# Performance work log

Measured on AMD Instinct MI355X. Metric: run time of the kernel, lower is better.

The kernel has to match this reference:

```python
import jax, jax.numpy as jnp
import numpy as np

N = 50000      # nodes
E = 800000     # edges (before self loops)
IN = 128       # input_dim
H1, C1 = 4, 64   # conv1 heads, per-head channels (concat -> 256)
H2, C2 = 1, 64   # conv2 heads, per-head channels (concat=False -> 64)
EPS_BN = 1e-5
NEG_SLOPE = 0.2


def setup_inputs() -> dict:
    key = jax.random.key(0)
    ks = jax.random.split(key, 20)
    s = 0.05
    d = {}
    d["x"] = jax.random.normal(ks[0], (N, IN), dtype=jnp.float32)
    d["edge_index"] = jax.random.randint(ks[1], (2, E), 0, N, dtype=jnp.int32)
    # GATConv 1: lin weight [IN, H1*C1], att vectors [H1, C1], bias [H1*C1]
    d["W1"] = jax.random.normal(ks[2], (IN, H1 * C1), dtype=jnp.float32) * s
    d["a1_src"] = jax.random.normal(ks[3], (H1, C1), dtype=jnp.float32) * s
    d["a1_dst"] = jax.random.normal(ks[4], (H1, C1), dtype=jnp.float32) * s
    d["b1"] = jnp.zeros((H1 * C1,), jnp.float32)
    # GATConv 2 (concat=False): lin weight [H1*C1, H2*C2]
    d["W2"] = jax.random.normal(ks[5], (H1 * C1, H2 * C2), dtype=jnp.float32) * s
    d["a2_src"] = jax.random.normal(ks[6], (H2, C2), dtype=jnp.float32) * s
    d["a2_dst"] = jax.random.normal(ks[7], (H2, C2), dtype=jnp.float32) * s
    d["b2"] = jnp.zeros((C2,), jnp.float32)
    # projection Linear(output_dim -> input_dim)
    d["Wp"] = jax.random.normal(ks[8], (C2, IN), dtype=jnp.float32) * s
    d["bp"] = jnp.zeros((IN,), jnp.float32)
    # BatchNorm affine params
    d["g1"] = jnp.ones((H1 * C1,), jnp.float32); d["be1"] = jnp.zeros((H1 * C1,), jnp.float32)
    d["g2"] = jnp.ones((C2,), jnp.float32);      d["be2"] = jnp.zeros((C2,), jnp.float32)
    d["g3"] = jnp.ones((IN,), jnp.float32);      d["be3"] = jnp.zeros((IN,), jnp.float32)
    return d


def batch_norm(x, gamma, beta):
    mu = jnp.mean(x, axis=0, keepdims=True)
    var = jnp.var(x, axis=0, keepdims=True)
    return (x - mu) * jax.lax.rsqrt(var + EPS_BN) * gamma + beta


def gat_conv(x, src, dst, W, a_src, a_dst, bias, heads, out_ch, concat):
    n = x.shape[0]
    h = (x @ W).reshape(n, heads, out_ch)            # [N,H,C]
    alpha_s = jnp.einsum('nhc,hc->nh', h, a_src)     # [N,H]
    alpha_d = jnp.einsum('nhc,hc->nh', h, a_dst)
    e = jax.nn.leaky_relu(alpha_s[src] + alpha_d[dst], NEG_SLOPE)  # [E',H]
    # segment softmax over edges sharing the same destination node
    m = jax.ops.segment_max(e, dst, num_segments=n)
    m = jnp.where(jnp.isfinite(m), m, 0.0)
    ex = jnp.exp(e - m[dst])
    den = jax.ops.segment_sum(ex, dst, num_segments=n)
    alpha = ex / (den[dst] + 1e-16)                  # [E',H]
    msg = alpha[:, :, None] * h[src]                 # [E',H,C]
    out = jax.ops.segment_sum(msg, dst, num_segments=n)  # [N,H,C]
    if concat:
        out = out.reshape(n, heads * out_ch)
    else:
        out = out.mean(axis=1)
    return out + bias


def reference(x, edge_index, W1, a1_src, a1_dst, b1, W2, a2_src, a2_dst, b2,
              Wp, bp, g1, be1, g2, be2, g3, be3):
    n = x.shape[0]
    # PyG GATConv default add_self_loops=True
    loops = jnp.arange(n, dtype=edge_index.dtype)
    src = jnp.concatenate([edge_index[0], loops])
    dst = jnp.concatenate([edge_index[1], loops])
    h = gat_conv(x, src, dst, W1, a1_src, a1_dst, b1, H1, C1, True)
    h = jax.nn.elu(batch_norm(h, g1, be1))
    # dropout is a no-op in eval mode
    h = gat_conv(h, src, dst, W2, a2_src, a2_dst, b2, H2, C2, False)
    h = jax.nn.elu(batch_norm(h, g2, be2))
    h = h @ Wp + bp
    return batch_norm(h, g3, be3)
```

## Files before the change

kernel.cpp:

```cpp
#include <hip/hip_runtime.h>
#include <cstdint>
#include <cstddef>

#define NEG_SLOPE 0.2f
#define EPS_BN 1e-5f

typedef __bf16 bf16x8 __attribute__((ext_vector_type(8)));
typedef float  f32x4  __attribute__((ext_vector_type(4)));
typedef float  f32x2  __attribute__((ext_vector_type(2)));
typedef unsigned short ushort_t;

static __device__ __forceinline__ float lrelu(float x){ return x > 0.f ? x : NEG_SLOPE * x; }
static __device__ __forceinline__ float elu(float x){ return x > 0.f ? x : __expf(x) - 1.f; }

static __device__ __forceinline__ ushort_t f2bf(float f){
  unsigned u = __float_as_uint(f);
  u += 0x7fffu + ((u >> 16) & 1u);
  return (ushort_t)(u >> 16);
}
static __device__ __forceinline__ void unpk(unsigned u, float& lo, float& hi){
  lo = __uint_as_float(u << 16);
  hi = __uint_as_float(u & 0xffff0000u);
}
static __device__ __forceinline__ f32x2 unpk2(unsigned u){
  f32x2 r;
  r.x = __uint_as_float(u << 16);
  r.y = __uint_as_float(u & 0xffff0000u);
  return r;
}

union BF8 { bf16x8 v; ushort_t u[8]; };

static inline int ceil_div(int a, int b){ return (a + b - 1) / b; }


static __device__ void packW_body(const float* W, ushort_t* Wp, int K, int Nn, int idx){
  int lane = idx & 63;
  int rest = idx >> 6;
  int KS = K >> 5;
  int s = rest % KS, t = rest / KS;
  int n  = t * 16 + (lane & 15);
  int k0 = s * 32 + (lane >> 4) * 8;
  ushort_t tmp[8];
  #pragma unroll
  for(int j = 0; j < 8; j++) tmp[j] = f2bf(W[(size_t)(k0 + j) * Nn + n]);
  uint4 pk;
  pk.x = tmp[0] | ((unsigned)tmp[1] << 16);
  pk.y = tmp[2] | ((unsigned)tmp[3] << 16);
  pk.z = tmp[4] | ((unsigned)tmp[5] << 16);
  pk.w = tmp[6] | ((unsigned)tmp[7] << 16);
  *reinterpret_cast<uint4*>(Wp + (size_t)idx * 8) = pk;
}

__global__ void init_kernel(unsigned* __restrict__ zbase, int ztotal,
                            const float* __restrict__ W1, const float* __restrict__ W2,
                            const float* __restrict__ W3, ushort_t* __restrict__ W1p,
                            ushort_t* __restrict__ W2p, ushort_t* __restrict__ W3p){
  int b = blockIdx.x;
  if(b < 28){
    int idx = b * 256 + threadIdx.x;
    if(idx < 4096)       packW_body(W1, W1p, 128, 256, idx);
    else if(idx < 6144)  packW_body(W2, W2p, 256, 64,  idx - 4096);
    else if(idx < 7168)  packW_body(W3, W3p, 64,  128, idx - 6144);
  } else {
    int i = (b - 28) * 256 + threadIdx.x;
    if(i < ztotal) zbase[i] = 0u;
  }
}


template<int K, int NT, int AMODE, int H>
static __device__ __forceinline__ void gemm_body(int bx, const void* __restrict__ Asrc,
                                                 const ushort_t* __restrict__ Bp,
                                                 ushort_t* __restrict__ C, int M,
                                                 const float* __restrict__ scale,
                                                 const float* __restrict__ shift,
                                                 const float* __restrict__ a_src,
                                                 const float* __restrict__ a_dst,
                                                 float* __restrict__ as_,
                                                 float* __restrict__ ad_){
  constexpr int KS = K >> 5;
  int lane = threadIdx.x & 63, wv = threadIdx.x >> 6;
  int row0 = bx * 64 + wv * 16;
  int mi = lane & 15, q = lane >> 4;
  int arow = row0 + mi; if(arow > M - 1) arow = M - 1;
  const bf16x8* bbase = reinterpret_cast<const bf16x8*>(Bp) + lane;
  f32x4 acc[NT] = {};
  #pragma unroll
  for(int s = 0; s < KS; s++){
    BF8 cv;
    if(AMODE == 0){
      const float* ap = (const float*)Asrc + (size_t)arow * K + s * 32 + q * 8;
      float4 u0 = *reinterpret_cast<const float4*>(ap);
      float4 u1 = *reinterpret_cast<const float4*>(ap + 4);
      cv.u[0] = f2bf(u0.x); cv.u[1] = f2bf(u0.y); cv.u[2] = f2bf(u0.z); cv.u[3] = f2bf(u0.w);
      cv.u[4] = f2bf(u1.x); cv.u[5] = f2bf(u1.y); cv.u[6] = f2bf(u1.z); cv.u[7] = f2bf(u1.w);
    } else {
      const ushort_t* ap = (const ushort_t*)Asrc + (size_t)arow * K + s * 32 + q * 8;
      uint4 u = *reinterpret_cast<const uint4*>(ap);
      int c0 = s * 32 + q * 8;
      float4 sc0 = *reinterpret_cast<const float4*>(scale + c0);
      float4 sc1 = *reinterpret_cast<const float4*>(scale + c0 + 4);
      float4 sh0 = *reinterpret_cast<const float4*>(shift + c0);
      float4 sh1 = *reinterpret_cast<const float4*>(shift + c0 + 4);
      float a, b;
      unpk(u.x, a, b); cv.u[0] = f2bf(elu(a * sc0.x + sh0.x)); cv.u[1] = f2bf(elu(b * sc0.y + sh0.y));
      unpk(u.y, a, b); cv.u[2] = f2bf(elu(a * sc0.z + sh0.z)); cv.u[3] = f2bf(elu(b * sc0.w + sh0.w));
      unpk(u.z, a, b); cv.u[4] = f2bf(elu(a * sc1.x + sh1.x)); cv.u[5] = f2bf(elu(b * sc1.y + sh1.y));
      unpk(u.w, a, b); cv.u[6] = f2bf(elu(a * sc1.z + sh1.z)); cv.u[7] = f2bf(elu(b * sc1.w + sh1.w));
    }
    bf16x8 af = cv.v;
    #pragma unroll
    for(int t = 0; t < NT; t++){
      bf16x8 bfr = bbase[((size_t)t * KS + s) * 64];
      acc[t] = __builtin_amdgcn_mfma_f32_16x16x32_bf16(af, bfr, acc[t], 0, 0, 0);
    }
  }
  #pragma unroll
  for(int t = 0; t < NT; t++){
    #pragma unroll
    for(int r = 0; r < 4; r++){
      int gr = row0 + q * 4 + r;
      if(gr < M) C[(size_t)gr * (NT * 16) + t * 16 + mi] = f2bf(acc[t][r]);
    }
  }
  if(H > 0){
    #pragma unroll
    for(int hh = 0; hh < H; hh++){
      #pragma unroll
      for(int r = 0; r < 4; r++){
        float ps = 0.f, pd = 0.f;
        #pragma unroll
        for(int tt = 0; tt < 4; tt++){
          int t = hh * 4 + tt;
          float av = acc[t][r];
          int c = t * 16 + mi;
          ps += av * a_src[c];
          pd += av * a_dst[c];
        }
        #pragma unroll
        for(int off = 1; off < 16; off <<= 1){
          ps += __shfl_xor(ps, off);
          pd += __shfl_xor(pd, off);
        }
        int gr = row0 + q * 4 + r;
        if(mi == 0 && gr < M){
          as_[(size_t)gr * H + hh] = ps;
          ad_[(size_t)gr * H + hh] = pd;
        }
      }
    }
  }
}

template<int K, int NT, int AMODE, int H>
__global__ __launch_bounds__(256) void gemm_kernel(const void* __restrict__ Asrc,
                                                   const ushort_t* __restrict__ Bp,
                                                   ushort_t* __restrict__ C, int M,
                                                   const float* __restrict__ scale,
                                                   const float* __restrict__ shift,
                                                   const float* __restrict__ a_src,
                                                   const float* __restrict__ a_dst,
                                                   float* __restrict__ as_,
                                                   float* __restrict__ ad_){
  gemm_body<K, NT, AMODE, H>(blockIdx.x, Asrc, Bp, C, M, scale, shift, a_src, a_dst, as_, ad_);
}

__global__ __launch_bounds__(256) void hist_gemm1_kernel(int GB, const int* __restrict__ ei,
                                                         int* __restrict__ deg, int E, int N,
                                                         const float* __restrict__ x,
                                                         const ushort_t* __restrict__ W1p,
                                                         ushort_t* __restrict__ h1b,
                                                         const float* __restrict__ a1s,
                                                         const float* __restrict__ a1d,
                                                         float* __restrict__ as_,
                                                         float* __restrict__ ad_){
  int b = blockIdx.x;
  if(b < GB){
    gemm_body<128, 16, 0, 4>(b, x, W1p, h1b, N, nullptr, nullptr, a1s, a1d, as_, ad_);
  } else {
    int e = (b - GB) * 256 + threadIdx.x;
    if(e < E + N){
      int d = (e < E) ? ei[E + e] : (e - E);
      atomicAdd(&deg[d], 1);
    }
  }
}


__global__ __launch_bounds__(256) void scan1_kernel(const int* __restrict__ deg, int* __restrict__ rowptr,
                                                    int* __restrict__ partials,
                                                    unsigned* __restrict__ tick, int n){
  int t = threadIdx.x, lane = t & 63, wv = t >> 6;
  int base = blockIdx.x * 2048 + t * 8;
  int v[8]; int run = 0;
  #pragma unroll
  for(int k = 0; k < 8; k++){ int i = base + k; v[k] = (i < n) ? deg[i] : 0; run += v[k]; }
  int sc = run;
  #pragma unroll
  for(int off = 1; off < 64; off <<= 1){
    int u = __shfl_up(sc, off);
    if(lane >= off) sc += u;
  }
  __shared__ int wtot[4], woff[4];
  __shared__ bool slast;
  if(lane == 63) wtot[wv] = sc;
  __syncthreads();
  if(t == 0){
    int a = 0;
    #pragma unroll
    for(int i = 0; i < 4; i++){ woff[i] = a; a += wtot[i]; }
    partials[blockIdx.x] = a;
  }
  __syncthreads();
  int excl = (sc - run) + woff[wv];
  #pragma unroll
  for(int k = 0; k < 8; k++){
    int i = base + k;
    if(i < n){ rowptr[i] = excl; excl += v[k]; }
  }
  if(t == 0){
    __threadfence();
    slast = (atomicAdd(tick, 1u) == (unsigned)(gridDim.x - 1));
  }
  __syncthreads();
  if(slast && t < 64){
    int nb = gridDim.x;
    int pv = (t < nb) ? atomicAdd(&partials[t], 0) : 0;
    int psc = pv;
    #pragma unroll
    for(int off = 1; off < 64; off <<= 1){
      int u = __shfl_up(psc, off);
      if(t >= off) psc += u;
    }
    if(t < nb) partials[t] = psc - pv;
  }
}

__global__ void scatter_kernel(const int* __restrict__ ei, int* __restrict__ rowptr,
                               const int* __restrict__ part, int* __restrict__ col, int E, int N){
  int e = blockIdx.x * 256 + threadIdx.x;
  if(e >= E + N) return;
  int s, d;
  if(e < E){ s = ei[e]; d = ei[E + e]; } else { s = e - E; d = e - E; }
  int pos = atomicAdd(&rowptr[d], 1) + part[d >> 11];
  col[pos] = s;
}


__global__ __launch_bounds__(256) void gat_agg4_kernel(const ushort_t* __restrict__ hfeat,
                                                       const float* __restrict__ as_,
                                                       const float* __restrict__ ad_,
                                                       const int* __restrict__ rowptr,
                                                       const int* __restrict__ part,
                                                       const int* __restrict__ col,
                                                       const float* __restrict__ bias,
                                                       ushort_t* __restrict__ out, int N){
  int wid = threadIdx.x >> 6, lane = threadIdx.x & 63;
  int n = blockIdx.x * 4 + wid;
  if(n > N - 1) n = N - 1;
  int start = n ? rowptr[n - 1] + part[(n - 1) >> 11] : 0;
  int end   = rowptr[n] + part[n >> 11];
  int g = lane >> 5, l = lane & 31, hidx = l >> 3;
  float adh = ad_[(size_t)n * 4 + hidx];
  float den = 0.f;
  f32x2 acc2[4] = {};
  auto body = [&](int j){
    int s = col[j];
    float w = __expf(lrelu(as_[(size_t)s * 4 + hidx] + adh));
    uint4 u = *reinterpret_cast<const uint4*>(hfeat + (size_t)s * 256 + 8 * l);
    den += w;
    acc2[0] += unpk2(u.x) * w;
    acc2[1] += unpk2(u.y) * w;
    acc2[2] += unpk2(u.z) * w;
    acc2[3] += unpk2(u.w) * w;
  };
  int j = start + g;
  for(; j + 6 < end; j += 8){ body(j); body(j + 2); body(j + 4); body(j + 6); }
  for(; j < end; j += 2) body(j);
  den += __shfl_xor(den, 32);
  #pragma unroll
  for(int k = 0; k < 4; k++){
    acc2[k].x += __shfl_xor(acc2[k].x, 32);
    acc2[k].y += __shfl_xor(acc2[k].y, 32);
  }
  float dinv = 1.f / (den + 1e-16f);
  int cbase = 8 * l + g * 4;
  f32x2 p0 = g ? acc2[2] : acc2[0];
  f32x2 p1 = g ? acc2[3] : acc2[1];
  ushort_t o0 = f2bf(p0.x * dinv + bias[cbase + 0]);
  ushort_t o1 = f2bf(p0.y * dinv + bias[cbase + 1]);
  ushort_t o2 = f2bf(p1.x * dinv + bias[cbase + 2]);
  ushort_t o3 = f2bf(p1.y * dinv + bias[cbase + 3]);
  uint2 pk; pk.x = o0 | ((unsigned)o1 << 16); pk.y = o2 | ((unsigned)o3 << 16);
  *reinterpret_cast<uint2*>(out + (size_t)n * 256 + cbase) = pk;
}


__global__ __launch_bounds__(256) void gat_agg1_kernel(const ushort_t* __restrict__ hfeat,
                                                       const float* __restrict__ as_,
                                                       const float* __restrict__ ad_,
                                                       const int* __restrict__ rowptr,
                                                       const int* __restrict__ part,
                                                       const int* __restrict__ col,
                                                       const float* __restrict__ bias,
                                                       ushort_t* __restrict__ out, int N){
  int wid = threadIdx.x >> 6, lane = threadIdx.x & 63;
  int n = blockIdx.x * 4 + wid;
  if(n > N - 1) n = N - 1;
  int start = n ? rowptr[n - 1] + part[(n - 1) >> 11] : 0;
  int end   = rowptr[n] + part[n >> 11];
  int g = lane >> 4, l = lane & 15;
  float adn = ad_[n];
  float den = 0.f;
  f32x2 acc2[2] = {};
  auto body = [&](int j){
    int s = col[j];
    float w = __expf(lrelu(as_[s] + adn));
    uint2 u = *reinterpret_cast<const uint2*>(hfeat + (size_t)s * 64 + 4 * l);
    den += w;
    acc2[0] += unpk2(u.x) * w;
    acc2[1] += unpk2(u.y) * w;
  };
  int j = start + g;
  for(; j + 4 < end; j += 8){ body(j); body(j + 4); }
  if(j < end) body(j);
  den += __shfl_xor(den, 16); den += __shfl_xor(den, 32);
  #pragma unroll
  for(int k = 0; k < 2; k++){
    acc2[k].x += __shfl_xor(acc2[k].x, 16); acc2[k].x += __shfl_xor(acc2[k].x, 32);
    acc2[k].y += __shfl_xor(acc2[k].y, 16); acc2[k].y += __shfl_xor(acc2[k].y, 32);
  }
  float dinv = 1.f / (den + 1e-16f);
  if(g == 0){
    ushort_t o0 = f2bf(acc2[0].x * dinv + bias[4 * l + 0]);
    ushort_t o1 = f2bf(acc2[0].y * dinv + bias[4 * l + 1]);
    ushort_t o2 = f2bf(acc2[1].x * dinv + bias[4 * l + 2]);
    ushort_t o3 = f2bf(acc2[1].y * dinv + bias[4 * l + 3]);
    uint2 pk; pk.x = o0 | ((unsigned)o1 << 16); pk.y = o2 | ((unsigned)o3 << 16);
    *reinterpret_cast<uint2*>(out + (size_t)n * 64 + 4 * l) = pk;
  }
}


template<int C>
__global__ __launch_bounds__(256) void colstats_fin_kernel(const ushort_t* __restrict__ x, int N,
                                                           float* __restrict__ stats,
                                                           const float* __restrict__ gamma,
                                                           const float* __restrict__ beta,
                                                           float* __restrict__ scale,
                                                           float* __restrict__ shift,
                                                           unsigned* __restrict__ ticket, int nblk){
  constexpr int TPR = C / 8;
  constexpr int RPB = 256 / TPR;
  int t = threadIdx.x;
  int c0 = (t % TPR) * 8, rg = t / TPR;
  float sum[8] = {}, sq[8] = {};
  for(int r = blockIdx.x * RPB + rg; r < N; r += gridDim.x * RPB){
    uint4 u = *reinterpret_cast<const uint4*>(x + (size_t)r * C + c0);
    float a, b;
    unpk(u.x, a, b); sum[0] += a; sq[0] += a * a; sum[1] += b; sq[1] += b * b;
    unpk(u.y, a, b); sum[2] += a; sq[2] += a * a; sum[3] += b; sq[3] += b * b;
    unpk(u.z, a, b); sum[4] += a; sq[4] += a * a; sum[5] += b; sq[5] += b * b;
    unpk(u.w, a, b); sum[6] += a; sq[6] += a * a; sum[7] += b; sq[7] += b * b;
  }
  __shared__ float red[2][256][8];
  #pragma unroll
  for(int k = 0; k < 8; k++){ red[0][t][k] = sum[k]; red[1][t][k] = sq[k]; }
  __syncthreads();
  if(t < C){
    int tr = t >> 3, k = t & 7;
    float S = 0.f, Q = 0.f;
    for(int g2 = 0; g2 < RPB; g2++){
      S += red[0][g2 * TPR + tr][k];
      Q += red[1][g2 * TPR + tr][k];
    }
    atomicAdd(&stats[t], S);
    atomicAdd(&stats[C + t], Q);
  }
  __shared__ bool is_last;
  __syncthreads();
  if(t == 0){
    __threadfence();
    is_last = (atomicAdd(ticket, 1u) == (unsigned)(nblk - 1));
  }
  __syncthreads();
  if(is_last && t < C){
    float S = atomicAdd(&stats[t], 0.f);
    float Q = atomicAdd(&stats[C + t], 0.f);
    float invN = 1.f / (float)N;
    float mu = S * invN;
    float var = Q * invN - mu * mu;
    float rs = rsqrtf(var + EPS_BN);
    float scl = rs * gamma[t];
    scale[t] = scl;
    shift[t] = beta[t] - mu * scl;
  }
}


__global__ void bn3_kernel(const ushort_t* __restrict__ x, const float* __restrict__ scale,
                           const float* __restrict__ shift, float* __restrict__ y, long total8){
  long i = (long)blockIdx.x * 256 + threadIdx.x;
  if(i >= total8) return;
  long e0 = i * 8;
  int c0 = (int)(e0 & 127);
  uint4 u = *reinterpret_cast<const uint4*>(x + e0);
  float4 sc0 = *reinterpret_cast<const float4*>(scale + c0);
  float4 sc1 = *reinterpret_cast<const float4*>(scale + c0 + 4);
  float4 sh0 = *reinterpret_cast<const float4*>(shift + c0);
  float4 sh1 = *reinterpret_cast<const float4*>(shift + c0 + 4);
  float a, b;
  float4 o0, o1;
  unpk(u.x, a, b); o0.x = a * sc0.x + sh0.x; o0.y = b * sc0.y + sh0.y;
  unpk(u.y, a, b); o0.z = a * sc0.z + sh0.z; o0.w = b * sc0.w + sh0.w;
  unpk(u.z, a, b); o1.x = a * sc1.x + sh1.x; o1.y = b * sc1.y + sh1.y;
  unpk(u.w, a, b); o1.z = a * sc1.z + sh1.z; o1.w = b * sc1.w + sh1.w;
  *reinterpret_cast<float4*>(y + e0) = o0;
  *reinterpret_cast<float4*>(y + e0 + 4) = o1;
}


extern "C" void kernel_launch(void* const* d_in, const int* in_sizes, int n_in,
                              void* d_out, int out_size, void* d_ws, size_t ws_size,
                              hipStream_t stream){
  const float* x   = (const float*)d_in[0];
  const int*   ei  = (const int*)  d_in[1];
  const float* W1  = (const float*)d_in[2];
  const float* a1s = (const float*)d_in[3];
  const float* a1d = (const float*)d_in[4];
  const float* b1  = (const float*)d_in[5];
  const float* W2  = (const float*)d_in[6];
  const float* a2s = (const float*)d_in[7];
  const float* a2d = (const float*)d_in[8];
  const float* b2  = (const float*)d_in[9];
  const float* Wp  = (const float*)d_in[10];
  const float* g1  = (const float*)d_in[12]; const float* be1 = (const float*)d_in[13];
  const float* g2  = (const float*)d_in[14]; const float* be2 = (const float*)d_in[15];
  const float* g3  = (const float*)d_in[16]; const float* be3 = (const float*)d_in[17];
  float* out = (float*)d_out;

  const int N  = in_sizes[0] / 128;
  const int E  = in_sizes[1] / 2;
  const int EP = E + N;
  const int Mpad = ((N + 63) / 64) * 64;
  const int NB = ceil_div(N, 2048);
  const int GB = Mpad / 64;
  const int HB = ceil_div(EP, 256);

  char* p = (char*)d_ws;
  auto carve = [&](size_t bytes) -> char* {
    char* r = p; p += (bytes + 255) & ~(size_t)255; return r;
  };
  float* meta   = (float*)carve(2048 * 4);
  int*   deg    = (int*)carve((size_t)N * 4);
  int*   rowptr = (int*)carve((size_t)(N + 1) * 4);
  int*   col    = (int*)carve((size_t)EP * 4);
  int*   part   = (int*)carve(64 * 4);
  float* as_    = (float*)carve((size_t)N * 4 * 4);
  float* ad_    = (float*)carve((size_t)N * 4 * 4);
  ushort_t* W1p = (ushort_t*)carve((size_t)128 * 256 * 2);
  ushort_t* W2p = (ushort_t*)carve((size_t)256 * 64 * 2);
  ushort_t* W3p = (ushort_t*)carve((size_t)64 * 128 * 2);
  ushort_t* h1b   = (ushort_t*)carve((size_t)Mpad * 256 * 2);
  ushort_t* out1b = (ushort_t*)carve((size_t)Mpad * 256 * 2);
  ushort_t* h2b   = (ushort_t*)carve((size_t)Mpad * 64 * 2);
  ushort_t* out2b = (ushort_t*)carve((size_t)Mpad * 64 * 2);
  ushort_t* h3b   = (ushort_t*)carve((size_t)Mpad * 128 * 2);

  float* stats1 = meta;        float* scale1 = meta + 512;  float* shift1 = meta + 768;
  float* stats2 = meta + 1024; float* scale2 = meta + 1152; float* shift2 = meta + 1216;
  float* stats3 = meta + 1280; float* scale3 = meta + 1536; float* shift3 = meta + 1664;
  unsigned* tick = (unsigned*)(meta + 1792);

  init_kernel<<<28 + ceil_div(2048 + N, 256), 256, 0, stream>>>((unsigned*)meta, 2048 + N,
                                                                W1, W2, Wp, W1p, W2p, W3p);
  hist_gemm1_kernel<<<GB + HB, 256, 0, stream>>>(GB, ei, deg, E, N, x, W1p, h1b, a1s, a1d, as_, ad_);
  scan1_kernel<<<NB, 256, 0, stream>>>(deg, rowptr, part, tick + 3, N);
  scatter_kernel<<<HB, 256, 0, stream>>>(ei, rowptr, part, col, E, N);
  gat_agg4_kernel<<<ceil_div(N, 4), 256, 0, stream>>>(h1b, as_, ad_, rowptr, part, col, b1, out1b, N);
  colstats_fin_kernel<256><<<512, 256, 0, stream>>>(out1b, N, stats1, g1, be1, scale1, shift1, tick + 0, 512);
  gemm_kernel<256, 4, 1, 1><<<GB, 256, 0, stream>>>(out1b, W2p, h2b, N, scale1, shift1, a2s, a2d, as_, ad_);
  gat_agg1_kernel<<<ceil_div(N, 4), 256, 0, stream>>>(h2b, as_, ad_, rowptr, part, col, b2, out2b, N);
  colstats_fin_kernel<64><<<512, 256, 0, stream>>>(out2b, N, stats2, g2, be2, scale2, shift2, tick + 1, 512);
  gemm_kernel<64, 8, 1, 0><<<GB, 256, 0, stream>>>(out2b, W3p, h3b, N, scale2, shift2, nullptr, nullptr, nullptr, nullptr);
  colstats_fin_kernel<128><<<512, 256, 0, stream>>>(h3b, N, stats3, g3, be3, scale3, shift3, tick + 2, 512);
  bn3_kernel<<<ceil_div(N * 16, 256), 256, 0, stream>>>(h3b, scale3, shift3, out, (long)N * 16);
}
```

Baseline: 417.0 us.

## Privatize degree histogram and scatter cursors into eight slices

```diff
diff --git a/kernel.cpp b/kernel.cpp
--- a/kernel.cpp
+++ b/kernel.cpp
@@ -167,7 +167,7 @@
 }
 
 __global__ __launch_bounds__(256) void hist_gemm1_kernel(int GB, const int* __restrict__ ei,
-                                                         int* __restrict__ deg, int E, int N,
+                                                         int* __restrict__ deg8, int E, int N,
                                                          const float* __restrict__ x,
                                                          const ushort_t* __restrict__ W1p,
                                                          ushort_t* __restrict__ h1b,
@@ -179,23 +179,31 @@
   if(b < GB){
     gemm_body<128, 16, 0, 4>(b, x, W1p, h1b, N, nullptr, nullptr, a1s, a1d, as_, ad_);
   } else {
-    int e = (b - GB) * 256 + threadIdx.x;
+    int hb = b - GB;
+    int e = hb * 256 + threadIdx.x;
     if(e < E + N){
       int d = (e < E) ? ei[E + e] : (e - E);
-      atomicAdd(&deg[d], 1);
-    }
-  }
-}
-
-
-__global__ __launch_bounds__(256) void scan1_kernel(const int* __restrict__ deg, int* __restrict__ rowptr,
+      atomicAdd(&deg8[(size_t)(hb & 7) * N + d], 1);
+    }
+  }
+}
+
+
+__global__ __launch_bounds__(256) void scan1_kernel(int* __restrict__ deg8, int* __restrict__ rowptr,
                                                     int* __restrict__ partials,
                                                     unsigned* __restrict__ tick, int n){
   int t = threadIdx.x, lane = t & 63, wv = t >> 6;
   int base = blockIdx.x * 2048 + t * 8;
   int v[8]; int run = 0;
   #pragma unroll
-  for(int k = 0; k < 8; k++){ int i = base + k; v[k] = (i < n) ? deg[i] : 0; run += v[k]; }
+  for(int k = 0; k < 8; k++){
+    int i = base + k; int s = 0;
+    if(i < n){
+      #pragma unroll
+      for(int r = 0; r < 8; r++) s += deg8[(size_t)r * n + i];
+    }
+    v[k] = s; run += s;
+  }
   int sc = run;
   #pragma unroll
   for(int off = 1; off < 64; off <<= 1){
@@ -217,7 +225,17 @@
   #pragma unroll
   for(int k = 0; k < 8; k++){
     int i = base + k;
-    if(i < n){ rowptr[i] = excl; excl += v[k]; }
+    if(i < n){
+      int run2 = excl;
+      #pragma unroll
+      for(int r = 0; r < 8; r++){
+        int tmp = deg8[(size_t)r * n + i];
+        deg8[(size_t)r * n + i] = run2;
+        run2 += tmp;
+      }
+      excl = run2;
+      rowptr[i] = excl;
+    }
   }
   if(t == 0){
     __threadfence();
@@ -237,13 +255,13 @@
   }
 }
 
-__global__ void scatter_kernel(const int* __restrict__ ei, int* __restrict__ rowptr,
+__global__ void scatter_kernel(const int* __restrict__ ei, int* __restrict__ cur8,
                                const int* __restrict__ part, int* __restrict__ col, int E, int N){
   int e = blockIdx.x * 256 + threadIdx.x;
   if(e >= E + N) return;
   int s, d;
   if(e < E){ s = ei[e]; d = ei[E + e]; } else { s = e - E; d = e - E; }
-  int pos = atomicAdd(&rowptr[d], 1) + part[d >> 11];
+  int pos = atomicAdd(&cur8[(size_t)(blockIdx.x & 7) * N + d], 1) + part[d >> 11];
   col[pos] = s;
 }
 
@@ -453,7 +471,7 @@
     char* r = p; p += (bytes + 255) & ~(size_t)255; return r;
   };
   float* meta   = (float*)carve(2048 * 4);
-  int*   deg    = (int*)carve((size_t)N * 4);
+  int*   deg8   = (int*)carve((size_t)8 * N * 4);
   int*   rowptr = (int*)carve((size_t)(N + 1) * 4);
   int*   col    = (int*)carve((size_t)EP * 4);
   int*   part   = (int*)carve(64 * 4);
@@ -473,11 +491,12 @@
   float* stats3 = meta + 1280; float* scale3 = meta + 1536; float* shift3 = meta + 1664;
   unsigned* tick = (unsigned*)(meta + 1792);
 
-  init_kernel<<<28 + ceil_div(2048 + N, 256), 256, 0, stream>>>((unsigned*)meta, 2048 + N,
-                                                                W1, W2, Wp, W1p, W2p, W3p);
-  hist_gemm1_kernel<<<GB + HB, 256, 0, stream>>>(GB, ei, deg, E, N, x, W1p, h1b, a1s, a1d, as_, ad_);
-  scan1_kernel<<<NB, 256, 0, stream>>>(deg, rowptr, part, tick + 3, N);
-  scatter_kernel<<<HB, 256, 0, stream>>>(ei, rowptr, part, col, E, N);
+  const int ZT = 2048 + 8 * N;
+  init_kernel<<<28 + ceil_div(ZT, 256), 256, 0, stream>>>((unsigned*)meta, ZT,
+                                                          W1, W2, Wp, W1p, W2p, W3p);
+  hist_gemm1_kernel<<<GB + HB, 256, 0, stream>>>(GB, ei, deg8, E, N, x, W1p, h1b, a1s, a1d, as_, ad_);
+  scan1_kernel<<<NB, 256, 0, stream>>>(deg8, rowptr, part, tick + 3, N);
+  scatter_kernel<<<HB, 256, 0, stream>>>(ei, deg8, part, col, E, N);
   gat_agg4_kernel<<<ceil_div(N, 4), 256, 0, stream>>>(h1b, as_, ad_, rowptr, part, col, b1, out1b, N);
   colstats_fin_kernel<256><<<512, 256, 0, stream>>>(out1b, N, stats1, g1, be1, scale1, shift1, tick + 0, 512);
   gemm_kernel<256, 4, 1, 1><<<GB, 256, 0, stream>>>(out1b, W2p, h2b, N, scale1, shift1, a2s, a2d, as_, ad_);
```

Measured after the change: 426.8 us. 2.3% more time.
